# Kernel optimization log

Hardware: AMD Instinct MI355X
Metric: run time of the kernel (lower is better)

## Reference

```python
import jax, jax.numpy as jnp
import numpy as np

B, T, C, H = 2, 2048, 1024, 16
D = C // H  # head dim = 64


def setup_inputs() -> dict:
    key = jax.random.key(0)
    ks = jax.random.split(key, 5)
    s = 0.02
    return {
        "x": jax.random.normal(ks[0], (B, T, C), dtype=jnp.float32),
        "c_attn_w": jax.random.normal(ks[1], (C, 3 * C), dtype=jnp.float32) * s,
        "c_attn_b": jax.random.normal(ks[2], (3 * C,), dtype=jnp.float32) * s,
        "c_proj_w": jax.random.normal(ks[3], (C, C), dtype=jnp.float32) * s,
        "c_proj_b": jax.random.normal(ks[4], (C,), dtype=jnp.float32) * s,
    }


def reference(x, c_attn_w, c_attn_b, c_proj_w, c_proj_b):
    b, t, c = x.shape
    # GPT-2 Conv1D: x @ W + b
    qkv = x @ c_attn_w + c_attn_b                      # [B,T,3C]
    q, k, v = jnp.split(qkv, 3, axis=-1)
    # [B,H,T,D]
    q = q.reshape(b, t, H, D).transpose(0, 2, 1, 3)
    k = k.reshape(b, t, H, D).transpose(0, 2, 1, 3)
    v = v.reshape(b, t, H, D).transpose(0, 2, 1, 3)
    scale = 1.0 / jnp.sqrt(jnp.float32(D))
    scores = jnp.einsum("bhqd,bhkd->bhqk", q, k) * scale  # [B,H,T,T]
    causal = jnp.tril(jnp.ones((t, t), dtype=bool))
    scores = jnp.where(causal, scores, jnp.float32(-jnp.inf))
    attn = jax.nn.softmax(scores, axis=-1)
    # drop_rate = 0.0 -> dropout is identity
    y = jnp.einsum("bhqk,bhkd->bhqd", attn, v)          # [B,H,T,D]
    y = y.transpose(0, 2, 1, 3).reshape(b, t, c)
    return y @ c_proj_w + c_proj_b
```

## Files before the change

### kernel.cpp

```cpp
#include <hip/hip_runtime.h>

#define B_ 2
#define T_ 2048
#define C_ 1024
#define H_ 16
#define D_ 64
#define M_ (B_ * T_)
#define NQKV_ (3 * C_)
#define NSEG_ 40

typedef unsigned short us16;
typedef unsigned int u32;
typedef short bf16x8 __attribute__((ext_vector_type(8)));
typedef float f32x4 __attribute__((ext_vector_type(4)));

__device__ __forceinline__ f32x4 mfma16(bf16x8 a, bf16x8 b, f32x4 c) {
    return __builtin_amdgcn_mfma_f32_16x16x32_bf16(a, b, c, 0, 0, 0);
}

__device__ __forceinline__ us16 f2bf(float f) {
    union { float f; u32 u; } v; v.f = f;
    u32 r = v.u + 0x7fffu + ((v.u >> 16) & 1u);
    return (us16)(r >> 16);
}
__device__ __forceinline__ u32 fbits(float f) {
    union { float f; u32 u; } v; v.f = f; return v.u;
}

typedef __attribute__((address_space(1))) const void as1_cvoid;
typedef __attribute__((address_space(3))) void as3_void;
__device__ __forceinline__ void gload_lds16(const us16* g, us16* l) {
    __builtin_amdgcn_global_load_lds((as1_cvoid*)g, (as3_void*)l, 16, 0, 0);
}

#define SCALE_LOG2E 0.1803368801111729f

__global__ __launch_bounds__(256) void cvt_bf16(
    const float* __restrict__ in, us16* __restrict__ out, int n8)
{
    const int i = blockIdx.x * blockDim.x + threadIdx.x;
    if (i >= n8) return;
    const float4 a = ((const float4*)in)[2 * i];
    const float4 b = ((const float4*)in)[2 * i + 1];
    ushort4 lo = { f2bf(a.x), f2bf(a.y), f2bf(a.z), f2bf(a.w) };
    ushort4 hi = { f2bf(b.x), f2bf(b.y), f2bf(b.z), f2bf(b.w) };
    ((ushort4*)out)[2 * i] = lo;
    ((ushort4*)out)[2 * i + 1] = hi;
}

__global__ __launch_bounds__(256) void transpose_cvt(
    const float* __restrict__ W, us16* __restrict__ Wt, int K, int N)
{
    __shared__ float tile[32][33];
    const int n0 = blockIdx.x * 32, k0 = blockIdx.y * 32;
    const int t = threadIdx.x;
    {
        const int k = t >> 3, n4 = (t & 7) * 4;
        const float4 v = *(const float4*)(W + (size_t)(k0 + k) * N + n0 + n4);
        tile[k][n4 + 0] = v.x; tile[k][n4 + 1] = v.y;
        tile[k][n4 + 2] = v.z; tile[k][n4 + 3] = v.w;
    }
    __syncthreads();
    {
        const int n = t >> 3, k4 = (t & 7) * 4;
        ushort4 o = { f2bf(tile[k4 + 0][n]), f2bf(tile[k4 + 1][n]),
                      f2bf(tile[k4 + 2][n]), f2bf(tile[k4 + 3][n]) };
        *(ushort4*)(Wt + (size_t)(n0 + n) * K + k0 + k4) = o;
    }
}

__global__ __launch_bounds__(256) void gemm_bf16(
    const us16* __restrict__ A, const us16* __restrict__ Bt,
    const float* __restrict__ bias, void* __restrict__ Cout,
    int M, int N, int K, int out_bf16)
{
    __shared__ __align__(16) us16 smem[17408];
    us16* sA = smem;
    us16* sB = smem + 128 * 64;

    const int tid = threadIdx.x;
    const int lane = tid & 63, wave = tid >> 6;
    const int wr = wave >> 1, wc = wave & 1;
    const int cq = lane & 15, quad = lane >> 4;
    const int m0 = blockIdx.y * 128, n0 = blockIdx.x * 128;

    const int srow = lane >> 3;
    const int schunk = (lane & 7) ^ srow;

    f32x4 acc[4][4];
    #pragma unroll
    for (int i = 0; i < 4; ++i)
        #pragma unroll
        for (int j = 0; j < 4; ++j)
            acc[i][j] = (f32x4){0.f, 0.f, 0.f, 0.f};

    for (int k0 = 0; k0 < K; k0 += 64) {
        #pragma unroll
        for (int i = 0; i < 4; ++i) {
            const int r0 = wave * 32 + i * 8;
            gload_lds16(A + (size_t)(m0 + r0 + srow) * K + k0 + schunk * 8,
                        sA + r0 * 64);
            gload_lds16(Bt + (size_t)(n0 + r0 + srow) * K + k0 + schunk * 8,
                        sB + r0 * 64);
        }
        __syncthreads();

        #pragma unroll
        for (int kk = 0; kk < 64; kk += 32) {
            const int cb = kk >> 3;
            bf16x8 af[4], bfg[4];
            #pragma unroll
            for (int i = 0; i < 4; ++i) {
                const int ra = wr * 64 + i * 16 + cq;
                af[i] = *(const bf16x8*)(sA + ra * 64 + (((cb + quad) ^ (cq & 7)) * 8));
                const int rb = wc * 64 + i * 16 + cq;
                bfg[i] = *(const bf16x8*)(sB + rb * 64 + (((cb + quad) ^ (cq & 7)) * 8));
            }
            #pragma unroll
            for (int mi = 0; mi < 4; ++mi)
                #pragma unroll
                for (int ni = 0; ni < 4; ++ni)
                    acc[mi][ni] = mfma16(af[mi], bfg[ni], acc[mi][ni]);
        }
        __syncthreads();
    }

    if (out_bf16) {
        const float sc = (n0 < 1024) ? SCALE_LOG2E : 1.0f;
        us16* Cs = smem;
        #pragma unroll
        for (int mi = 0; mi < 4; ++mi)
            #pragma unroll
            for (int ni = 0; ni < 4; ++ni) {
                const int n = n0 + wc * 64 + ni * 16 + cq;
                const float bv = bias[n];
                #pragma unroll
                for (int r = 0; r < 4; ++r)
                    Cs[(wr * 64 + mi * 16 + quad * 4 + r) * 136 +
                       wc * 64 + ni * 16 + cq] = f2bf((acc[mi][ni][r] + bv) * sc);
            }
        __syncthreads();
        us16* Co = (us16*)Cout;
        #pragma unroll
        for (int p = 0; p < 8; ++p) {
            const int chunk = p * 256 + tid;
            const int r = chunk >> 4, c = (chunk & 15) * 8;
            *(uint4*)(Co + (size_t)(m0 + r) * N + n0 + c) =
                *(const uint4*)(Cs + r * 136 + c);
        }
    } else {
        float* Co = (float*)Cout;
        #pragma unroll
        for (int mi = 0; mi < 4; ++mi)
            #pragma unroll
            for (int ni = 0; ni < 4; ++ni) {
                const int n = n0 + wc * 64 + ni * 16 + cq;
                const float bv = bias[n];
                #pragma unroll
                for (int r = 0; r < 4; ++r)
                    Co[(size_t)(m0 + wr * 64 + mi * 16 + quad * 4 + r) * N + n] =
                        acc[mi][ni][r] + bv;
            }
    }
}

__global__ __launch_bounds__(128) void attn_mfma(
    const us16* __restrict__ qkv, float* __restrict__ Opart,
    float* __restrict__ Lpart)
{
    __shared__ __align__(16) us16 Ks[64 * 64];
    __shared__ __align__(16) us16 Vt[64 * 64];
    __shared__ __align__(16) us16 Ps[128 * 64];

    const int tid = threadIdx.x;
    const int lane = tid & 63, wave = tid >> 6;
    const int cq = lane & 15, quad = lane >> 4;

    const int f = blockIdx.x;
    const int bh = f & 31;
    const int u = (NSEG_ - 1) - (f >> 5);
    int qb = 15, off = 0;
    for (int i = 0; i < 16; ++i) {
        const int ns = (2 * i + 9) >> 3;
        if (u < off + ns) { qb = i; break; }
        off += ns;
    }
    const int seg = u - off;
    const int slot = bh * NSEG_ + off + seg;
    const int b = bh >> 4, h = bh & 15;

    const us16* base = qkv + (size_t)b * T_ * NQKV_ + h * D_;

    bf16x8 qf[4][2];
    #pragma unroll
    for (int qs = 0; qs < 4; ++qs) {
        const us16* qrow = base +
            (size_t)(qb * 128 + wave * 64 + qs * 16 + cq) * NQKV_;
        qf[qs][0] = *(const bf16x8*)(qrow + quad * 8);
        qf[qs][1] = *(const bf16x8*)(qrow + 32 + quad * 8);
    }

    f32x4 o[4][4];
    #pragma unroll
    for (int qs = 0; qs < 4; ++qs)
        #pragma unroll
        for (int dt = 0; dt < 4; ++dt)
            o[qs][dt] = (f32x4){0.f, 0.f, 0.f, 0.f};
    float l[4] = {0.f, 0.f, 0.f, 0.f};

    const int srow = lane >> 3;
    const int schunk = (lane & 7) ^ srow;
    const int t2 = tid & 31, dg = tid >> 5;
    const int kt_lo = seg * 8;
    const int kt_hi = min(seg * 8 + 7, 2 * qb + 1);

    for (int kt = kt_lo; kt <= kt_hi; ++kt) {
        __syncthreads();

        #pragma unroll
        for (int i = 0; i < 4; ++i) {
            const int r0 = wave * 32 + i * 8;
            gload_lds16(base + (size_t)(kt * 64 + r0 + srow) * NQKV_ + C_ + schunk * 8,
                        Ks + r0 * 64);
        }
        #pragma unroll
        for (int half = 0; half < 2; ++half) {
            const int dbase = dg * 16 + half * 8;
            const us16* vp = base + (size_t)(kt * 64 + 2 * t2) * NQKV_ + 2 * C_ + dbase;
            const uint4 u0 = *(const uint4*)vp;
            const uint4 u1 = *(const uint4*)(vp + NQKV_);
            const us16* p0 = (const us16*)&u0;
            const us16* p1 = (const us16*)&u1;
            #pragma unroll
            for (int j = 0; j < 8; ++j) {
                const int d = dbase + j;
                const u32 pk = (u32)p0[j] | ((u32)p1[j] << 16);
                *(u32*)(Vt + d * 64 + (((t2 >> 2) ^ (d & 7)) * 8) + (t2 & 3) * 2) = pk;
            }
        }
        __syncthreads();

        if (kt <= 2 * qb + wave) {
            const bool diag = (kt == 2 * qb + wave);

            bf16x8 kf[4][2];
            #pragma unroll
            for (int j = 0; j < 4; ++j)
                #pragma unroll
                for (int ds = 0; ds < 2; ++ds)
                    kf[j][ds] = *(const bf16x8*)(Ks + (j * 16 + cq) * 64 +
                                  (((ds * 4 + quad) ^ (cq & 7)) * 8));

            #pragma unroll
            for (int qs = 0; qs < 4; ++qs) {
                f32x4 s[4];
                #pragma unroll
                for (int j = 0; j < 4; ++j) {
                    f32x4 t = (f32x4){0.f, 0.f, 0.f, 0.f};
                    t = mfma16(kf[j][0], qf[qs][0], t);
                    t = mfma16(kf[j][1], qf[qs][1], t);
                    s[j] = t;
                }
                if (diag) {
                    const int qg = qb * 128 + wave * 64 + qs * 16 + cq;
                    const int kb = kt * 64;
                    #pragma unroll
                    for (int j = 0; j < 4; ++j)
                        #pragma unroll
                        for (int r = 0; r < 4; ++r)
                            if (kb + j * 16 + quad * 4 + r > qg) s[j][r] = -1e30f;
                }
                float sum = 0.f;
                #pragma unroll
                for (int j = 0; j < 4; ++j)
                    #pragma unroll
                    for (int r = 0; r < 4; ++r) {
                        s[j][r] = exp2f(s[j][r]);
                        sum += s[j][r];
                    }
                l[qs] += sum;
                const int prow = wave * 64 + qs * 16 + cq;
                #pragma unroll
                for (int j = 0; j < 4; ++j) {
                    uint2 w;
                    w.x = (fbits(s[j][1]) & 0xffff0000u) | (fbits(s[j][0]) >> 16);
                    w.y = (fbits(s[j][3]) & 0xffff0000u) | (fbits(s[j][2]) >> 16);
                    *(uint2*)(Ps + prow * 64 +
                              (((2 * j + (quad >> 1)) ^ (cq & 7)) * 8) +
                              (quad & 1) * 4) = w;
                }
            }

            bf16x8 vf[4][2];
            #pragma unroll
            for (int dt = 0; dt < 4; ++dt)
                #pragma unroll
                for (int ks = 0; ks < 2; ++ks)
                    vf[dt][ks] = *(const bf16x8*)(Vt + (dt * 16 + cq) * 64 +
                                   (((ks * 4 + quad) ^ (cq & 7)) * 8));
            #pragma unroll
            for (int qs = 0; qs < 4; ++qs) {
                const int prow = wave * 64 + qs * 16 + cq;
                const bf16x8 pf0 = *(const bf16x8*)(Ps + prow * 64 +
                                     ((quad ^ (cq & 7)) * 8));
                const bf16x8 pf1 = *(const bf16x8*)(Ps + prow * 64 +
                                     (((4 + quad) ^ (cq & 7)) * 8));
                #pragma unroll
                for (int dt = 0; dt < 4; ++dt) {
                    o[qs][dt] = mfma16(pf0, vf[dt][0], o[qs][dt]);
                    o[qs][dt] = mfma16(pf1, vf[dt][1], o[qs][dt]);
                }
            }
        }
    }

    float* Ob = Opart + (size_t)slot * (128 * 64);
    #pragma unroll
    for (int qs = 0; qs < 4; ++qs) {
        float lt = l[qs];
        lt += __shfl_xor(lt, 16);
        lt += __shfl_xor(lt, 32);
        if (quad == 0)
            Lpart[slot * 128 + wave * 64 + qs * 16 + cq] = lt;
        #pragma unroll
        for (int r = 0; r < 4; ++r) {
            const int qloc = wave * 64 + qs * 16 + quad * 4 + r;
            #pragma unroll
            for (int dt = 0; dt < 4; ++dt)
                Ob[qloc * 64 + dt * 16 + cq] = o[qs][dt][r];
        }
    }
}

__global__ __launch_bounds__(128) void attn_combine(
    const float* __restrict__ Opart, const float* __restrict__ Lpart,
    us16* __restrict__ yb)
{
    const int bh = blockIdx.x, qb = blockIdx.y, q = threadIdx.x;
    int off = 0;
    for (int i = 0; i < qb; ++i) off += (2 * i + 9) >> 3;
    const int ns = (2 * qb + 9) >> 3;
    const int s0 = bh * NSEG_ + off;

    float L = 0.f;
    for (int s = 0; s < ns; ++s) L += Lpart[(s0 + s) * 128 + q];
    const float inv = 1.0f / L;

    const int b = bh >> 4, h = bh & 15;
    us16* yrow = yb + (size_t)(b * T_ + qb * 128 + q) * C_ + h * D_;
    #pragma unroll
    for (int d4 = 0; d4 < 16; ++d4) {
        float4 a = {0.f, 0.f, 0.f, 0.f};
        for (int s = 0; s < ns; ++s) {
            const float4 v = *(const float4*)(Opart +
                (size_t)(s0 + s) * (128 * 64) + q * 64 + d4 * 4);
            a.x += v.x; a.y += v.y; a.z += v.z; a.w += v.w;
        }
        ushort4 ov = { f2bf(a.x * inv), f2bf(a.y * inv),
                       f2bf(a.z * inv), f2bf(a.w * inv) };
        *(ushort4*)(yrow + d4 * 4) = ov;
    }
}

extern "C" void kernel_launch(void* const* d_in, const int* in_sizes, int n_in,
                              void* d_out, int out_size, void* d_ws, size_t ws_size,
                              hipStream_t stream)
{
    const float* x  = (const float*)d_in[0];
    const float* aw = (const float*)d_in[1];
    const float* ab = (const float*)d_in[2];
    const float* pw = (const float*)d_in[3];
    const float* pb = (const float*)d_in[4];
    float* out = (float*)d_out;

    us16* xb    = (us16*)d_ws;
    us16* awT   = xb  + (size_t)M_ * C_;
    us16* pwT   = awT + (size_t)NQKV_ * C_;
    us16* qkvb  = pwT + (size_t)C_ * C_;
    us16* yb    = qkvb + (size_t)M_ * NQKV_;
    float* Opart = (float*)(yb + (size_t)M_ * C_);
    float* Lpart = Opart + (size_t)32 * NSEG_ * 128 * 64;

    cvt_bf16<<<(M_ * C_ / 8 + 255) / 256, 256, 0, stream>>>(x, xb, M_ * C_ / 8);
    transpose_cvt<<<dim3(NQKV_ / 32, C_ / 32), 256, 0, stream>>>(aw, awT, C_, NQKV_);
    transpose_cvt<<<dim3(C_ / 32, C_ / 32), 256, 0, stream>>>(pw, pwT, C_, C_);

    gemm_bf16<<<dim3(NQKV_ / 128, M_ / 128), 256, 0, stream>>>(
        xb, awT, ab, qkvb, M_, NQKV_, C_, 1);

    attn_mfma<<<dim3(32 * NSEG_), 128, 0, stream>>>(qkvb, Opart, Lpart);
    attn_combine<<<dim3(32, 16), 128, 0, stream>>>(Opart, Lpart, yb);

    gemm_bf16<<<dim3(C_ / 128, M_ / 128), 256, 0, stream>>>(
        yb, pwT, pb, out, M_, C_, C_, 0);
}
```

Before: 241.7 us.

## Pre-transpose V in QKV GEMM epilogue and double-buffer K/V attention loads

The QKV GEMM epilogue now writes the V columns into a per-head transposed [bh][d][t] buffer. This lets the attention kernel fetch V with async global-to-LDS loads instead of doing a scalar register transpose on every tile. K and V tiles are double-buffered in LDS, so the next tile is prefetched while the current one is computed, and one barrier per iteration is dropped. The partial-output buffer is also stored d-major with vector stores, and the combine kernel reads it coalesced into 64 register accumulators, which raises register pressure. The y buffer now shares memory with the V-transposed buffer.

```diff
diff --git a/kernel.cpp b/kernel.cpp
--- a/kernel.cpp
+++ b/kernel.cpp
@@ -72,7 +72,7 @@
 __global__ __launch_bounds__(256) void gemm_bf16(
     const us16* __restrict__ A, const us16* __restrict__ Bt,
     const float* __restrict__ bias, void* __restrict__ Cout,
-    int M, int N, int K, int out_bf16)
+    us16* __restrict__ vt, int M, int N, int K, int out_bf16)
 {
     __shared__ __align__(16) us16 smem[17408];
     us16* sA = smem;
@@ -140,13 +140,30 @@
                        wc * 64 + ni * 16 + cq] = f2bf((acc[mi][ni][r] + bv) * sc);
             }
         __syncthreads();
-        us16* Co = (us16*)Cout;
-        #pragma unroll
-        for (int p = 0; p < 8; ++p) {
-            const int chunk = p * 256 + tid;
-            const int r = chunk >> 4, c = (chunk & 15) * 8;
-            *(uint4*)(Co + (size_t)(m0 + r) * N + n0 + c) =
-                *(const uint4*)(Cs + r * 136 + c);
+        if (vt && n0 >= 2048) {
+            const int c = tid & 127;
+            const int half = tid >> 7;
+            const int bh = (m0 >> 11) * 16 + ((n0 - 2048) >> 6) + (c >> 6);
+            const int d = c & 63;
+            const int t0 = (m0 & 2047) + half * 64;
+            us16* vrow = vt + (size_t)bh * (64 * 2048) + (size_t)d * 2048 + t0;
+            #pragma unroll
+            for (int w = 0; w < 8; ++w) {
+                union { uint4 v; us16 e[8]; } pk;
+                #pragma unroll
+                for (int j = 0; j < 8; ++j)
+                    pk.e[j] = Cs[(half * 64 + w * 8 + j) * 136 + c];
+                *(uint4*)(vrow + w * 8) = pk.v;
+            }
+        } else {
+            us16* Co = (us16*)Cout;
+            #pragma unroll
+            for (int p = 0; p < 8; ++p) {
+                const int chunk = p * 256 + tid;
+                const int r = chunk >> 4, c = (chunk & 15) * 8;
+                *(uint4*)(Co + (size_t)(m0 + r) * N + n0 + c) =
+                    *(const uint4*)(Cs + r * 136 + c);
+            }
         }
     } else {
         float* Co = (float*)Cout;
@@ -165,11 +182,11 @@
 }
 
 __global__ __launch_bounds__(128) void attn_mfma(
-    const us16* __restrict__ qkv, float* __restrict__ Opart,
-    float* __restrict__ Lpart)
-{
-    __shared__ __align__(16) us16 Ks[64 * 64];
-    __shared__ __align__(16) us16 Vt[64 * 64];
+    const us16* __restrict__ qkv, const us16* __restrict__ vt,
+    float* __restrict__ Opart, float* __restrict__ Lpart)
+{
+    __shared__ __align__(16) us16 sK[2][64 * 64];
+    __shared__ __align__(16) us16 sV[2][64 * 64];
     __shared__ __align__(16) us16 Ps[128 * 64];
 
     const int tid = threadIdx.x;
@@ -190,6 +207,8 @@
     const int b = bh >> 4, h = bh & 15;
 
     const us16* base = qkv + (size_t)b * T_ * NQKV_ + h * D_;
+    const us16* kq = base + C_;
+    const us16* vbh = vt + (size_t)bh * (64 * 2048);
 
     bf16x8 qf[4][2];
     #pragma unroll
@@ -210,45 +229,45 @@
 
     const int srow = lane >> 3;
     const int schunk = (lane & 7) ^ srow;
-    const int t2 = tid & 31, dg = tid >> 5;
     const int kt_lo = seg * 8;
     const int kt_hi = min(seg * 8 + 7, 2 * qb + 1);
 
+    #pragma unroll
+    for (int i = 0; i < 4; ++i) {
+        const int r0 = wave * 32 + i * 8;
+        gload_lds16(kq + (size_t)(kt_lo * 64 + r0 + srow) * NQKV_ + schunk * 8,
+                    &sK[0][r0 * 64]);
+        gload_lds16(vbh + (size_t)(r0 + srow) * 2048 + kt_lo * 64 + schunk * 8,
+                    &sV[0][r0 * 64]);
+    }
+
     for (int kt = kt_lo; kt <= kt_hi; ++kt) {
+        const int cur = (kt - kt_lo) & 1;
         __syncthreads();
 
-        #pragma unroll
-        for (int i = 0; i < 4; ++i) {
-            const int r0 = wave * 32 + i * 8;
-            gload_lds16(base + (size_t)(kt * 64 + r0 + srow) * NQKV_ + C_ + schunk * 8,
-                        Ks + r0 * 64);
+        if (kt < kt_hi) {
+            const int nb = cur ^ 1;
+            #pragma unroll
+            for (int i = 0; i < 4; ++i) {
+                const int r0 = wave * 32 + i * 8;
+                gload_lds16(kq + (size_t)((kt + 1) * 64 + r0 + srow) * NQKV_ + schunk * 8,
+                            &sK[nb][r0 * 64]);
+                gload_lds16(vbh + (size_t)(r0 + srow) * 2048 + (kt + 1) * 64 + schunk * 8,
+                            &sV[nb][r0 * 64]);
+            }
         }
-        #pragma unroll
-        for (int half = 0; half < 2; ++half) {
-            const int dbase = dg * 16 + half * 8;
-            const us16* vp = base + (size_t)(kt * 64 + 2 * t2) * NQKV_ + 2 * C_ + dbase;
-            const uint4 u0 = *(const uint4*)vp;
-            const uint4 u1 = *(const uint4*)(vp + NQKV_);
-            const us16* p0 = (const us16*)&u0;
-            const us16* p1 = (const us16*)&u1;
-            #pragma unroll
-            for (int j = 0; j < 8; ++j) {
-                const int d = dbase + j;
-                const u32 pk = (u32)p0[j] | ((u32)p1[j] << 16);
-                *(u32*)(Vt + d * 64 + (((t2 >> 2) ^ (d & 7)) * 8) + (t2 & 3) * 2) = pk;
-            }
-        }
-        __syncthreads();
 
         if (kt <= 2 * qb + wave) {
             const bool diag = (kt == 2 * qb + wave);
+            const us16* Kc = sK[cur];
+            const us16* Vc = sV[cur];
 
             bf16x8 kf[4][2];
             #pragma unroll
             for (int j = 0; j < 4; ++j)
                 #pragma unroll
                 for (int ds = 0; ds < 2; ++ds)
-                    kf[j][ds] = *(const bf16x8*)(Ks + (j * 16 + cq) * 64 +
+                    kf[j][ds] = *(const bf16x8*)(Kc + (j * 16 + cq) * 64 +
                                   (((ds * 4 + quad) ^ (cq & 7)) * 8));
 
             #pragma unroll
@@ -296,7 +315,7 @@
             for (int dt = 0; dt < 4; ++dt)
                 #pragma unroll
                 for (int ks = 0; ks < 2; ++ks)
-                    vf[dt][ks] = *(const bf16x8*)(Vt + (dt * 16 + cq) * 64 +
+                    vf[dt][ks] = *(const bf16x8*)(Vc + (dt * 16 + cq) * 64 +
                                    (((ks * 4 + quad) ^ (cq & 7)) * 8));
             #pragma unroll
             for (int qs = 0; qs < 4; ++qs) {
@@ -314,7 +333,7 @@
         }
     }
 
-    float* Ob = Opart + (size_t)slot * (128 * 64);
+    float* Ob = Opart + (size_t)slot * (64 * 128);
     #pragma unroll
     for (int qs = 0; qs < 4; ++qs) {
         float lt = l[qs];
@@ -323,12 +342,9 @@
         if (quad == 0)
             Lpart[slot * 128 + wave * 64 + qs * 16 + cq] = lt;
         #pragma unroll
-        for (int r = 0; r < 4; ++r) {
-            const int qloc = wave * 64 + qs * 16 + quad * 4 + r;
-            #pragma unroll
-            for (int dt = 0; dt < 4; ++dt)
-                Ob[qloc * 64 + dt * 16 + cq] = o[qs][dt][r];
-        }
+        for (int dt = 0; dt < 4; ++dt)
+            *(f32x4*)(Ob + (dt * 16 + cq) * 128 + wave * 64 + qs * 16 + quad * 4)
+                = o[qs][dt];
     }
 }
 
@@ -346,19 +362,23 @@
     for (int s = 0; s < ns; ++s) L += Lpart[(s0 + s) * 128 + q];
     const float inv = 1.0f / L;
 
+    float acc[64];
+    #pragma unroll
+    for (int d = 0; d < 64; ++d) acc[d] = 0.f;
+    for (int s = 0; s < ns; ++s) {
+        const float* Ob = Opart + (size_t)(s0 + s) * (64 * 128);
+        #pragma unroll
+        for (int d = 0; d < 64; ++d) acc[d] += Ob[d * 128 + q];
+    }
+
     const int b = bh >> 4, h = bh & 15;
     us16* yrow = yb + (size_t)(b * T_ + qb * 128 + q) * C_ + h * D_;
     #pragma unroll
-    for (int d4 = 0; d4 < 16; ++d4) {
-        float4 a = {0.f, 0.f, 0.f, 0.f};
-        for (int s = 0; s < ns; ++s) {
-            const float4 v = *(const float4*)(Opart +
-                (size_t)(s0 + s) * (128 * 64) + q * 64 + d4 * 4);
-            a.x += v.x; a.y += v.y; a.z += v.z; a.w += v.w;
-        }
-        ushort4 ov = { f2bf(a.x * inv), f2bf(a.y * inv),
-                       f2bf(a.z * inv), f2bf(a.w * inv) };
-        *(ushort4*)(yrow + d4 * 4) = ov;
+    for (int d8 = 0; d8 < 8; ++d8) {
+        union { uint4 v; us16 e[8]; } pk;
+        #pragma unroll
+        for (int j = 0; j < 8; ++j) pk.e[j] = f2bf(acc[d8 * 8 + j] * inv);
+        *(uint4*)(yrow + d8 * 8) = pk.v;
     }
 }
 
@@ -377,8 +397,9 @@
     us16* awT   = xb  + (size_t)M_ * C_;
     us16* pwT   = awT + (size_t)NQKV_ * C_;
     us16* qkvb  = pwT + (size_t)C_ * C_;
-    us16* yb    = qkvb + (size_t)M_ * NQKV_;
-    float* Opart = (float*)(yb + (size_t)M_ * C_);
+    us16* vt    = qkvb + (size_t)M_ * NQKV_;
+    us16* yb    = vt;
+    float* Opart = (float*)(vt + (size_t)32 * 64 * 2048);
     float* Lpart = Opart + (size_t)32 * NSEG_ * 128 * 64;
 
     cvt_bf16<<<(M_ * C_ / 8 + 255) / 256, 256, 0, stream>>>(x, xb, M_ * C_ / 8);
@@ -386,11 +407,11 @@
     transpose_cvt<<<dim3(C_ / 32, C_ / 32), 256, 0, stream>>>(pw, pwT, C_, C_);
 
     gemm_bf16<<<dim3(NQKV_ / 128, M_ / 128), 256, 0, stream>>>(
-        xb, awT, ab, qkvb, M_, NQKV_, C_, 1);
-
-    attn_mfma<<<dim3(32 * NSEG_), 128, 0, stream>>>(qkvb, Opart, Lpart);
+        xb, awT, ab, qkvb, vt, M_, NQKV_, C_, 1);
+
+    attn_mfma<<<dim3(32 * NSEG_), 128, 0, stream>>>(qkvb, vt, Opart, Lpart);
     attn_combine<<<dim3(32, 16), 128, 0, stream>>>(Opart, Lpart, yb);
 
     gemm_bf16<<<dim3(C_ / 128, M_ / 128), 256, 0, stream>>>(
-        yb, pwT, pb, out, M_, C_, C_, 0);
-}
+        yb, pwT, pb, out, nullptr, M_, C_, C_, 0);
+}
```

New measurement: 242.5 us. About the same (+0.3%).
